# Kernel tuning notes

Hardware: AMD Instinct MI355X
Metric: run time of the kernel (lower is better)

The kernel has to match this reference:

```python
import jax, jax.numpy as jnp
import numpy as np

N_NODES = 100000
LN_EPS = 1e-5
NEG_SLOPE = 0.2


def setup_inputs() -> dict:
    key = jax.random.key(0)
    ks = jax.random.split(key, 6)
    N, E, NIN, EDIM, NOUT, H = N_NODES, 1600000, 64, 32, 128, 4
    x = jax.random.normal(ks[0], (N, NIN), dtype=jnp.float32)
    edge_index = jax.random.randint(ks[1], (2, E), 0, N, dtype=jnp.int64)
    edge_attr = jax.random.normal(ks[2], (E, EDIM), dtype=jnp.float32)
    # xavier-uniform linear weights (torch layout: [out, in])
    def xavier(k, fan_out, fan_in):
        lim = float(np.sqrt(6.0 / (fan_in + fan_out)))
        return jax.random.uniform(k, (fan_out, fan_in), jnp.float32, -lim, lim)
    W_msg = xavier(ks[3], NOUT, NIN + EDIM)          # (128, 96)
    W_att = xavier(ks[4], H, 2 * NIN + EDIM)         # (4, 160)
    bias = jnp.zeros((NOUT,), jnp.float32)
    ln_gamma = jnp.ones((NOUT,), jnp.float32)
    ln_beta = jnp.zeros((NOUT,), jnp.float32)
    return {"x": x, "edge_index": edge_index, "edge_attr": edge_attr,
            "W_msg": W_msg, "W_att": W_att, "bias": bias,
            "ln_gamma": ln_gamma, "ln_beta": ln_beta}


def reference(x, edge_index, edge_attr, W_msg, W_att, bias, ln_gamma, ln_beta):
    N = x.shape[0]
    H = W_att.shape[0]
    src, dst = edge_index[0], edge_index[1]
    xs = x[src]                                       # (E, node_in) gather
    xd = x[dst]                                       # (E, node_in) gather
    # message: W_msg @ [h_u ; x_uv]
    msg_in = jnp.concatenate([xs, edge_attr], axis=-1)            # (E, 96)
    msgs = msg_in @ W_msg.T                                        # (E, out_dim)
    msgs = msgs.reshape(-1, H, W_msg.shape[0] // H)                # (E, H, D)
    # attention logits: LeakyReLU(W_att @ [h_u ; h_v ; x_uv])
    att_in = jnp.concatenate([xs, xd, edge_attr], axis=-1)         # (E, 160)
    logits = att_in @ W_att.T                                      # (E, H)
    logits = jax.nn.leaky_relu(logits, NEG_SLOPE)
    # per-destination-node sparse softmax
    seg_max = jax.ops.segment_max(logits, dst, num_segments=N)     # (N, H)
    exp_l = jnp.exp(logits - seg_max[dst])                         # (E, H)
    seg_sum = jax.ops.segment_sum(exp_l, dst, num_segments=N)      # (N, H)
    att = exp_l / (seg_sum[dst] + 1e-9)                            # (E, H)
    # weighted scatter-add aggregation
    weighted = msgs * att[..., None]                               # (E, H, D)
    out = jax.ops.segment_sum(weighted, dst, num_segments=N)       # (N, H, D)
    out = out.reshape(N, -1) + bias                                # concat heads
    # layer norm over feature dim
    mu = out.mean(axis=-1, keepdims=True)
    var = out.var(axis=-1, keepdims=True)
    out = (out - mu) * jax.lax.rsqrt(var + LN_EPS) * ln_gamma + ln_beta
    return out
```

## Files before the change

### kernel.cpp

```cpp
#include <hip/hip_runtime.h>
#include <hip/hip_bf16.h>

typedef __attribute__((ext_vector_type(8))) short short8;
typedef __attribute__((ext_vector_type(4))) float f32x4;

__device__ __forceinline__ unsigned short fbf(float f) {
  union { float f; unsigned u; } v; v.f = f;
  unsigned r = v.u + 0x7fffu + ((v.u >> 16) & 1u);
  return (unsigned short)(r >> 16);
}
__device__ __forceinline__ unsigned pk2(float a, float b) {
  return (unsigned)fbf(a) | ((unsigned)fbf(b) << 16);
}
__device__ __forceinline__ float ubf(unsigned hi) {
  union { unsigned u; float f; } v; v.u = hi << 16; return v.f;
}
__device__ __forceinline__ float ubf_lo(unsigned u) {
  union { unsigned u; float f; } v; v.u = u << 16; return v.f;
}
__device__ __forceinline__ float ubf_hi(unsigned u) {
  union { unsigned u; float f; } v; v.u = u & 0xffff0000u; return v.f;
}
__device__ __forceinline__ float dot4(float4 a, float4 b) {
  return fmaf(a.x, b.x, fmaf(a.y, b.y, fmaf(a.z, b.z, a.w * b.w)));
}

__launch_bounds__(256)
__global__ void k_phase1(const float* __restrict__ x, const float* __restrict__ W_att,
                         const int* __restrict__ edst, int E,
                         float4* __restrict__ A_s, float4* __restrict__ A_d,
                         unsigned* __restrict__ xb32, int* __restrict__ deg,
                         int* __restrict__ rank, int N) {
  __shared__ float4 s_wa[160];
  if (threadIdx.x < 160) s_wa[threadIdx.x] = ((const float4*)W_att)[threadIdx.x];
  for (int i = blockIdx.x * blockDim.x + threadIdx.x; i < E; i += gridDim.x * blockDim.x)
    rank[i] = atomicAdd(&deg[edst[i]], 1);
  __syncthreads();
  for (int v = blockIdx.x * blockDim.x + threadIdx.x; v < N; v += gridDim.x * blockDim.x) {
    const float4* xp = (const float4*)&x[v * 64];
    float4 xq[16];
    #pragma unroll
    for (int k = 0; k < 16; k++) xq[k] = xp[k];
    float as[4] = {}, ad[4] = {};
    #pragma unroll
    for (int h = 0; h < 4; h++) {
      #pragma unroll
      for (int k = 0; k < 16; k++) {
        as[h] += dot4(s_wa[h * 40 + k], xq[k]);
        ad[h] += dot4(s_wa[h * 40 + 16 + k], xq[k]);
      }
    }
    A_s[v] = make_float4(as[0], as[1], as[2], as[3]);
    A_d[v] = make_float4(ad[0], ad[1], ad[2], ad[3]);
    #pragma unroll
    for (int k = 0; k < 16; k++) {
      xb32[v * 32 + 2 * k]     = pk2(xq[k].x, xq[k].y);
      xb32[v * 32 + 2 * k + 1] = pk2(xq[k].z, xq[k].w);
    }
  }
}

__global__ void k_scan1(const int* __restrict__ deg, int N, int* __restrict__ part,
                        int* __restrict__ bsum) {
  __shared__ int tmp[1024];
  int tid = threadIdx.x;
  int i = blockIdx.x * 1024 + tid;
  int dv = (i < N) ? deg[i] : 0;
  int v = (dv + 7) & ~7;
  tmp[tid] = v;
  __syncthreads();
  for (int ofs = 1; ofs < 1024; ofs <<= 1) {
    int t = (tid >= ofs) ? tmp[tid - ofs] : 0;
    __syncthreads();
    tmp[tid] += t;
    __syncthreads();
  }
  if (i < N) part[i] = tmp[tid] - v;
  if (tid == 1023) bsum[blockIdx.x] = tmp[tid];
}

__global__ void k_scan2(int* __restrict__ part, const int* __restrict__ bsum,
                        const int* __restrict__ deg, int N, int4* __restrict__ csrp) {
  __shared__ int sbase;
  if (threadIdx.x == 0) {
    int b = 0;
    for (int j = 0; j < (int)blockIdx.x; j++) b += bsum[j];
    sbase = b;
  }
  __syncthreads();
  int i = blockIdx.x * 1024 + threadIdx.x;
  if (i < N) {
    const int o = part[i] + sbase;
    part[i] = o;
    const int d = deg[i];
    const int pe = o + ((d + 7) & ~7);
    const int4 z = make_int4(0, 0, 0, 0);
    for (int s = o + d; s < pe; s++) csrp[s] = z;
    if (i == N - 1) part[N] = pe;
  }
}

__launch_bounds__(256)
__global__ void k_att2(const int* __restrict__ esrc, const int* __restrict__ edst, int E,
                       const float* __restrict__ ea, const float4* __restrict__ A_s,
                       const float4* __restrict__ A_d, const float* __restrict__ W_att,
                       uint2* __restrict__ att_eo) {
  __shared__ float4 s_we[32];
  if (threadIdx.x < 32) {
    int h = threadIdx.x >> 3, k4 = threadIdx.x & 7;
    const float* p = &W_att[h * 160 + 128 + k4 * 4];
    s_we[threadIdx.x] = make_float4(p[0], p[1], p[2], p[3]);
  }
  __syncthreads();
  for (int e = blockIdx.x * blockDim.x + threadIdx.x; e < E; e += gridDim.x * blockDim.x) {
    const int s = esrc[e], d = edst[e];
    const float4* ep = (const float4*)&ea[(unsigned)e * 32u];
    float4 eq[8];
    #pragma unroll
    for (int k = 0; k < 8; k++) eq[k] = ep[k];
    const float4 as4 = A_s[s], ad4 = A_d[d];
    const float base[4] = {as4.x + ad4.x, as4.y + ad4.y, as4.z + ad4.z, as4.w + ad4.w};
    float av[4];
    #pragma unroll
    for (int h = 0; h < 4; h++) {
      float lg = base[h];
      #pragma unroll
      for (int k = 0; k < 8; k++) lg += dot4(s_we[h * 8 + k], eq[k]);
      lg = fmaxf(lg, 0.2f * lg);
      av[h] = __expf(lg);
    }
    att_eo[e] = make_uint2(pk2(av[0], av[1]), pk2(av[2], av[3]));
  }
}

__launch_bounds__(256)
__global__ void k_scat(const int* __restrict__ esrc, const int* __restrict__ edst,
                       const int* __restrict__ rank, const int* __restrict__ offsets,
                       const uint2* __restrict__ att_eo, int E, int4* __restrict__ csrp) {
  for (int e = blockIdx.x * blockDim.x + threadIdx.x; e < E; e += gridDim.x * blockDim.x) {
    const int d = edst[e];
    const int slot = offsets[d] + rank[e];
    const uint2 a = att_eo[e];
    csrp[slot] = make_int4(esrc[e], e, (int)a.x, (int)a.y);
  }
}

__launch_bounds__(256)
__global__ void k_aggP(const unsigned short* __restrict__ xb, const float* __restrict__ ea,
                       const int4* __restrict__ csrp, const int* __restrict__ offsets,
                       unsigned short* __restrict__ agg, float* __restrict__ denom, int N) {
  __shared__ int4 s_ids[4][32];
  const int lane = threadIdx.x & 63;
  const int wvb = threadIdx.x >> 6;
  const int wv = (blockIdx.x * blockDim.x + threadIdx.x) >> 6;
  const int nw = (gridDim.x * blockDim.x) >> 6;
  const int l32 = lane & 31;
  const bool hi = lane >= 32;

  for (int v0 = wv; v0 < N; v0 += nw) {
    const int vv = __builtin_amdgcn_readfirstlane(v0);
    const int sstart = __builtin_amdgcn_readfirstlane(offsets[vv]);
    const int send = __builtin_amdgcn_readfirstlane(offsets[vv + 1]);
    const int ng = (send - sstart) >> 3;
    const int nq = (ng + 3) >> 2;

    float ax0 = 0, ax1 = 0, ax2 = 0, ax3 = 0;
    float ae0 = 0, ae1 = 0, ae2 = 0, ae3 = 0;
    float dn0 = 0, dn1 = 0, dn2 = 0, dn3 = 0;

    for (int q = 0; q < nq; q++) {
      {
        int4 q_ = csrp[sstart + q * 32 + l32];
        if (lane < 32) s_ids[wvb][l32] = q_;
      }
      const int nsc = min(4, ng - q * 4);
      float ev[4][8];
      unsigned short qv[4][8];
      #pragma unroll
      for (int sc = 0; sc < 4; sc++) {
        if (sc < nsc) {
          #pragma unroll
          for (int p = 0; p < 8; p++) {
            const int4 t_ = s_ids[wvb][sc * 8 + p];
            qv[sc][p] = xb[(unsigned)(t_.x << 6) + lane];
            ev[sc][p] = ea[(unsigned)(t_.y << 5) + l32];
          }
        }
      }
      #pragma unroll
      for (int sc = 0; sc < 4; sc++) {
        if (sc < nsc) {
          #pragma unroll
          for (int p = 0; p < 8; p++) {
            const int4 t_ = s_ids[wvb][sc * 8 + p];
            const float a0_ = ubf_lo((unsigned)t_.z);
            const float a1_ = ubf_hi((unsigned)t_.z);
            const float a2_ = ubf_lo((unsigned)t_.w);
            const float a3_ = ubf_hi((unsigned)t_.w);
            const float xf = ubf((unsigned)qv[sc][p]);
            const float evp = ev[sc][p];
            ax0 = fmaf(a0_, xf, ax0); ax1 = fmaf(a1_, xf, ax1);
            ax2 = fmaf(a2_, xf, ax2); ax3 = fmaf(a3_, xf, ax3);
            ae0 = fmaf(a0_, evp, ae0); ae1 = fmaf(a1_, evp, ae1);
            ae2 = fmaf(a2_, evp, ae2); ae3 = fmaf(a3_, evp, ae3);
            dn0 += a0_; dn1 += a1_; dn2 += a2_; dn3 += a3_;
          }
        }
      }
    }

    const unsigned base = (unsigned)v0 * 384u;
    agg[base + lane]        = fbf(ax0);
    agg[base + 96 + lane]   = fbf(ax1);
    agg[base + 192 + lane]  = fbf(ax2);
    agg[base + 288 + lane]  = fbf(ax3);
    const int hA = hi ? 2 : 0;
    agg[base + hA * 96 + 64 + l32]       = fbf(hi ? ae2 : ae0);
    agg[base + (hA + 1) * 96 + 64 + l32] = fbf(hi ? ae3 : ae1);
    if (lane == 0) ((float4*)denom)[v0] = make_float4(dn0, dn1, dn2, dn3);
  }
}

__launch_bounds__(128)
__global__ void k_out(const unsigned short* __restrict__ agg, const float* __restrict__ W_msg,
                      const float* __restrict__ denom, const float* __restrict__ bias,
                      const float* __restrict__ gamma, const float* __restrict__ beta,
                      float* __restrict__ out, int N, int T) {
  __shared__ float s_den[64];
  __shared__ float s_sum[2][16], s_sq[2][16];
  const int f = threadIdx.x;
  const int w = f >> 6;
  const int l = f & 63;
  const int c16 = l & 15;
  const int rg = l >> 4;

  short8 wb[2][2][3];
  float biasv[2][2], gv[2][2], bv[2][2];
  #pragma unroll
  for (int hh = 0; hh < 2; hh++) {
    const int head = 2 * w + hh;
    #pragma unroll
    for (int ct = 0; ct < 2; ct++) {
      const int q = head * 32 + ct * 16 + c16;
      biasv[hh][ct] = bias[q]; gv[hh][ct] = gamma[q]; bv[hh][ct] = beta[q];
      #pragma unroll
      for (int kk = 0; kk < 3; kk++) {
        const float* p = &W_msg[q * 96 + kk * 32 + rg * 8];
        short8 s;
        #pragma unroll
        for (int i = 0; i < 8; i++) s[i] = (short)fbf(p[i]);
        wb[hh][ct][kk] = s;
      }
    }
  }

  for (int t = blockIdx.x; t < T; t += gridDim.x) {
    const int n0 = t * 16;
    if (f < 64) s_den[f] = denom[min(n0 + (f >> 2), N - 1) * 4 + (f & 3)];
    __syncthreads();

    f32x4 c[2][2] = {{{0.f,0.f,0.f,0.f},{0.f,0.f,0.f,0.f}},
                     {{0.f,0.f,0.f,0.f},{0.f,0.f,0.f,0.f}}};
    const int nA = min(n0 + c16, N - 1);
    #pragma unroll
    for (int hh = 0; hh < 2; hh++) {
      const int head = 2 * w + hh;
      #pragma unroll
      for (int kk = 0; kk < 3; kk++) {
        short8 a = *(const short8*)&agg[nA * 384 + head * 96 + kk * 32 + rg * 8];
        c[hh][0] = __builtin_amdgcn_mfma_f32_16x16x32_bf16(a, wb[hh][0][kk], c[hh][0], 0, 0, 0);
        c[hh][1] = __builtin_amdgcn_mfma_f32_16x16x32_bf16(a, wb[hh][1][kk], c[hh][1], 0, 0, 0);
      }
    }

    float val[2][2][4];
    #pragma unroll
    for (int hh = 0; hh < 2; hh++)
      #pragma unroll
      for (int ct = 0; ct < 2; ct++)
        #pragma unroll
        for (int r = 0; r < 4; r++) {
          const float d = s_den[(rg * 4 + r) * 4 + (2 * w + hh)] + 1e-9f;
          val[hh][ct][r] = c[hh][ct][r] / d + biasv[hh][ct];
        }

    float sr[4], qr[4];
    #pragma unroll
    for (int r = 0; r < 4; r++) {
      float s = 0.f, q2 = 0.f;
      #pragma unroll
      for (int hh = 0; hh < 2; hh++)
        #pragma unroll
        for (int ct = 0; ct < 2; ct++) { s += val[hh][ct][r]; q2 = fmaf(val[hh][ct][r], val[hh][ct][r], q2); }
      #pragma unroll
      for (int m = 1; m <= 8; m <<= 1) { s += __shfl_xor(s, m, 64); q2 += __shfl_xor(q2, m, 64); }
      sr[r] = s; qr[r] = q2;
    }
    if (c16 == 0) {
      #pragma unroll
      for (int r = 0; r < 4; r++) { s_sum[w][rg * 4 + r] = sr[r]; s_sq[w][rg * 4 + r] = qr[r]; }
    }
    __syncthreads();

    float mean[4], rstd[4];
    #pragma unroll
    for (int r = 0; r < 4; r++) {
      const int ni = rg * 4 + r;
      mean[r] = (s_sum[0][ni] + s_sum[1][ni]) * (1.f / 128.f);
      const float m2 = (s_sq[0][ni] + s_sq[1][ni]) * (1.f / 128.f);
      rstd[r] = rsqrtf(m2 - mean[r] * mean[r] + 1e-5f);
    }
    #pragma unroll
    for (int hh = 0; hh < 2; hh++)
      #pragma unroll
      for (int ct = 0; ct < 2; ct++)
        #pragma unroll
        for (int r = 0; r < 4; r++) {
          const int n = n0 + rg * 4 + r;
          if (n < N)
            out[n * 128 + (2 * w + hh) * 32 + ct * 16 + c16] =
                (val[hh][ct][r] - mean[r]) * rstd[r] * gv[hh][ct] + bv[hh][ct];
        }
    __syncthreads();
  }
}

extern "C" void kernel_launch(void* const* d_in, const int* in_sizes, int n_in,
                              void* d_out, int out_size, void* d_ws, size_t ws_size,
                              hipStream_t stream) {
  const float* x     = (const float*)d_in[0];
  const int*   ei    = (const int*)d_in[1];
  const float* ea    = (const float*)d_in[2];
  const float* W_msg = (const float*)d_in[3];
  const float* W_att = (const float*)d_in[4];
  const float* bias  = (const float*)d_in[5];
  const float* gamma = (const float*)d_in[6];
  const float* beta  = (const float*)d_in[7];
  float* out = (float*)d_out;

  const int N = in_sizes[0] / 64;
  const int E = in_sizes[1] / 2;
  const int* esrc = ei;
  const int* edst = ei + E;
  const int EP = E + 8 * N + 64;

  char* p = (char*)d_ws;
  int* deg      = (int*)p;            p += (size_t)N * 4;
  int* offsets  = (int*)p;            p += (size_t)(N + 1) * 4;
  int* rank     = (int*)p;            p += (size_t)E * 4;
  int* bsum     = (int*)p;            p += 2048 * 4;
  int4* csrp    = (int4*)p;           p += (size_t)EP * 16;
  float4* A_s   = (float4*)p;         p += (size_t)N * 16;
  float4* A_d   = (float4*)p;         p += (size_t)N * 16;
  unsigned short* xb = (unsigned short*)p; p += (size_t)N * 64 * 2;
  unsigned short* agg = (unsigned short*)p; p += (size_t)N * 384 * 2;
  float* denom  = (float*)p;
  uint2* att_eo = (uint2*)agg;

  hipMemsetAsync(deg, 0, (size_t)N * 4, stream);
  const int SB = (N + 1023) / 1024;
  const int T = (N + 15) / 16;

  k_phase1<<<2048, 256, 0, stream>>>(x, W_att, edst, E, A_s, A_d, (unsigned*)xb, deg, rank, N);
  k_scan1<<<SB, 1024, 0, stream>>>(deg, N, offsets, bsum);
  k_scan2<<<SB, 1024, 0, stream>>>(offsets, bsum, deg, N, csrp);
  k_att2<<<2048, 256, 0, stream>>>(esrc, edst, E, ea, A_s, A_d, W_att, att_eo);
  k_scat<<<2048, 256, 0, stream>>>(esrc, edst, rank, offsets, att_eo, E, csrp);
  k_aggP<<<2048, 256, 0, stream>>>(xb, ea, csrp, offsets, agg, denom, N);
  k_out<<<T, 128, 0, stream>>>(agg, W_msg, denom, bias, gamma, beta, out, N, T);
}
```

Baseline: 396.5 us.

## Software-pipeline CSR index loads in aggregation kernel and enlarge grids

The aggregation kernel now double-buffers its per-wave shared index tile and prefetches the next 32-entry chunk of CSR records, including the first chunk of the next node, while the current chunk is gathered and accumulated. This hides the dependent index load latency that sat in front of each gather batch. Grid sizes for the attention, scatter and aggregation kernels are also doubled to 4096 blocks. The prefetch reads past the last node using a clamped index. It adds register and LDS pressure, and the single-buffer-per-iteration reuse relies on wave-synchronous execution.

```diff
diff --git a/kernel.cpp b/kernel.cpp
--- a/kernel.cpp
+++ b/kernel.cpp
@@ -149,7 +149,7 @@
 __global__ void k_aggP(const unsigned short* __restrict__ xb, const float* __restrict__ ea,
                        const int4* __restrict__ csrp, const int* __restrict__ offsets,
                        unsigned short* __restrict__ agg, float* __restrict__ denom, int N) {
-  __shared__ int4 s_ids[4][32];
+  __shared__ int4 s_ids[4][2][32];
   const int lane = threadIdx.x & 63;
   const int wvb = threadIdx.x >> 6;
   const int wv = (blockIdx.x * blockDim.x + threadIdx.x) >> 6;
@@ -157,22 +157,30 @@
   const int l32 = lane & 31;
   const bool hi = lane >= 32;
 
-  for (int v0 = wv; v0 < N; v0 += nw) {
-    const int vv = __builtin_amdgcn_readfirstlane(v0);
-    const int sstart = __builtin_amdgcn_readfirstlane(offsets[vv]);
-    const int send = __builtin_amdgcn_readfirstlane(offsets[vv + 1]);
+  if (wv >= N) return;
+
+  int v0 = wv;
+  int sstart = __builtin_amdgcn_readfirstlane(offsets[v0]);
+  int send   = __builtin_amdgcn_readfirstlane(offsets[v0 + 1]);
+  int4 pre = csrp[sstart + l32];
+  int buf = 0;
+
+  while (true) {
     const int ng = (send - sstart) >> 3;
     const int nq = (ng + 3) >> 2;
+    const int vn = v0 + nw;
+    const int vc = (vn < N) ? vn : (N - 1);
+    const int sstart_n = __builtin_amdgcn_readfirstlane(offsets[vc]);
+    const int send_n   = __builtin_amdgcn_readfirstlane(offsets[vc + 1]);
 
     float ax0 = 0, ax1 = 0, ax2 = 0, ax3 = 0;
     float ae0 = 0, ae1 = 0, ae2 = 0, ae3 = 0;
     float dn0 = 0, dn1 = 0, dn2 = 0, dn3 = 0;
 
     for (int q = 0; q < nq; q++) {
-      {
-        int4 q_ = csrp[sstart + q * 32 + l32];
-        if (lane < 32) s_ids[wvb][l32] = q_;
-      }
+      if (lane < 32) s_ids[wvb][buf][l32] = pre;
+      const int nbase = (q + 1 < nq) ? (sstart + (q + 1) * 32) : sstart_n;
+      pre = csrp[nbase + l32];
       const int nsc = min(4, ng - q * 4);
       float ev[4][8];
       unsigned short qv[4][8];
@@ -181,7 +189,7 @@
         if (sc < nsc) {
           #pragma unroll
           for (int p = 0; p < 8; p++) {
-            const int4 t_ = s_ids[wvb][sc * 8 + p];
+            const int4 t_ = s_ids[wvb][buf][sc * 8 + p];
             qv[sc][p] = xb[(unsigned)(t_.x << 6) + lane];
             ev[sc][p] = ea[(unsigned)(t_.y << 5) + l32];
           }
@@ -192,7 +200,7 @@
         if (sc < nsc) {
           #pragma unroll
           for (int p = 0; p < 8; p++) {
-            const int4 t_ = s_ids[wvb][sc * 8 + p];
+            const int4 t_ = s_ids[wvb][buf][sc * 8 + p];
             const float a0_ = ubf_lo((unsigned)t_.z);
             const float a1_ = ubf_hi((unsigned)t_.z);
             const float a2_ = ubf_lo((unsigned)t_.w);
@@ -207,7 +215,9 @@
           }
         }
       }
-    }
+      buf ^= 1;
+    }
+    if (nq == 0) pre = csrp[sstart_n + l32];
 
     const unsigned base = (unsigned)v0 * 384u;
     agg[base + lane]        = fbf(ax0);
@@ -218,6 +228,9 @@
     agg[base + hA * 96 + 64 + l32]       = fbf(hi ? ae2 : ae0);
     agg[base + (hA + 1) * 96 + 64 + l32] = fbf(hi ? ae3 : ae1);
     if (lane == 0) ((float4*)denom)[v0] = make_float4(dn0, dn1, dn2, dn3);
+
+    if (vn >= N) break;
+    v0 = vn; sstart = sstart_n; send = send_n;
   }
 }
 
@@ -364,8 +377,8 @@
   k_phase1<<<2048, 256, 0, stream>>>(x, W_att, edst, E, A_s, A_d, (unsigned*)xb, deg, rank, N);
   k_scan1<<<SB, 1024, 0, stream>>>(deg, N, offsets, bsum);
   k_scan2<<<SB, 1024, 0, stream>>>(offsets, bsum, deg, N, csrp);
-  k_att2<<<2048, 256, 0, stream>>>(esrc, edst, E, ea, A_s, A_d, W_att, att_eo);
-  k_scat<<<2048, 256, 0, stream>>>(esrc, edst, rank, offsets, att_eo, E, csrp);
-  k_aggP<<<2048, 256, 0, stream>>>(xb, ea, csrp, offsets, agg, denom, N);
+  k_att2<<<4096, 256, 0, stream>>>(esrc, edst, E, ea, A_s, A_d, W_att, att_eo);
+  k_scat<<<4096, 256, 0, stream>>>(esrc, edst, rank, offsets, att_eo, E, csrp);
+  k_aggP<<<4096, 256, 0, stream>>>(xb, ea, csrp, offsets, agg, denom, N);
   k_out<<<T, 128, 0, stream>>>(agg, W_msg, denom, bias, gamma, beta, out, N, T);
 }
```

After: 401.5 us. About the same (+1.3%).
